# Kernel tuning notes

Measured on AMD Instinct MI355X. Metric: run time of the kernel, lower is better.

Reference implementation:

```python
import jax, jax.numpy as jnp
import numpy as np

N_NODES = 50000
N_EDGES = 800000
IN_FEATS = 256
OUT_FEATS = 64


def setup_inputs() -> dict:
    key = jax.random.key(0)
    k1, k2, k3, k4 = jax.random.split(key, 4)
    feat = jax.random.normal(k1, (N_NODES, IN_FEATS), dtype=jnp.float32)
    # xavier_uniform-like init for weight
    limit = float(np.sqrt(6.0 / (IN_FEATS + OUT_FEATS)))
    weight = jax.random.uniform(k2, (IN_FEATS, OUT_FEATS), dtype=jnp.float32,
                                minval=-limit, maxval=limit)
    bias = jnp.zeros((OUT_FEATS,), dtype=jnp.float32)
    src = jax.random.randint(k3, (N_EDGES,), 0, N_NODES, dtype=jnp.int32)
    dst = jax.random.randint(k4, (N_EDGES,), 0, N_NODES, dtype=jnp.int32)
    return {"feat": feat, "weight": weight, "bias": bias, "src": src, "dst": dst}


def reference(feat, weight, bias, src, dst):
    # GCN GraphConv with norm='both', edge_weight=None, activation=None.
    n = feat.shape[0]
    ones_e = jnp.ones(src.shape[0], dtype=feat.dtype)
    out_deg = jnp.clip(jax.ops.segment_sum(ones_e, src, num_segments=n), 1.0)
    in_deg = jnp.clip(jax.ops.segment_sum(ones_e, dst, num_segments=n), 1.0)

    # left/both pre-normalization by out-degree^{-1/2}
    feat_src = feat * (out_deg ** -0.5)[:, None]

    # lin_before_mp: in_feats (256) > out_feats (64) -> project first
    h = feat_src @ weight  # [N, out_feats]

    # copy_u + sum aggregation: gather from src, scatter-add to dst
    rst = jax.ops.segment_sum(h[src], dst, num_segments=n)  # [N, out_feats]

    # right/both post-normalization by in-degree^{-1/2}, then bias
    rst = rst * (in_deg ** -0.5)[:, None] + bias
    return rst
```

## Files before the change

kernel.cpp:

```cpp
#include <hip/hip_runtime.h>
#include <hip/hip_bf16.h>

#define N_NODES 50000
#define N_EDGES 800000
#define IN_F 256
#define OUT_F 64
#define NBUCKET 196
#define CAPB 6144
#define HCOPIES 32
#define EDGES_PER_COPY 25000
#define HWORDS 25000
#define PBLOCKS 200
#define EDGES_PER_PBLOCK 4000

using bf16x8 = __attribute__((ext_vector_type(8))) short;
using f32x4  = __attribute__((ext_vector_type(4))) float;

__global__ __launch_bounds__(1024)
void hist_kernel(const int* __restrict__ src, unsigned* __restrict__ scratch) {
    __shared__ unsigned lh[HWORDS];
    int tid = threadIdx.x, b = blockIdx.x;
    int e0 = b * EDGES_PER_COPY;
    for (int i = tid; i < HWORDS; i += 1024) lh[i] = 0;
    __syncthreads();
    for (int i = tid; i < EDGES_PER_COPY; i += 1024) {
        int id = src[e0 + i];
        atomicAdd(&lh[id >> 1], (id & 1) ? 0x10000u : 1u);
    }
    __syncthreads();
    unsigned* outp = scratch + (size_t)b * HWORDS;
    for (int i = tid; i < HWORDS; i += 1024) outp[i] = lh[i];
}

__global__ void reduce_kernel(const unsigned* __restrict__ scratch,
                              int* __restrict__ cnt_out) {
    int j = blockIdx.x * blockDim.x + threadIdx.x;
    if (j >= HWORDS) return;
    unsigned lo = 0, hi = 0;
    for (int k = 0; k < HCOPIES; ++k) {
        unsigned v = scratch[(size_t)k * HWORDS + j];
        lo += v & 0xFFFFu; hi += v >> 16;
    }
    cnt_out[2 * j] = (int)lo;
    cnt_out[2 * j + 1] = (int)hi;
}

__global__ __launch_bounds__(1024)
void partition_kernel(const int* __restrict__ src, const int* __restrict__ dst,
                      int* __restrict__ bucket_cursor, unsigned* __restrict__ recs) {
    __shared__ int lcnt[NBUCKET], lbase[NBUCKET];
    int tid = threadIdx.x;
    int e0 = blockIdx.x * EDGES_PER_PBLOCK;
    if (tid < NBUCKET) lcnt[tid] = 0;
    __syncthreads();
    unsigned rec[4]; int bkt[4], rnk[4];
#pragma unroll
    for (int j = 0; j < 4; ++j) {
        int i = j * 1024 + tid;
        bkt[j] = -1;
        if (i < EDGES_PER_PBLOCK) {
            int e = e0 + i;
            int s = src[e], d = dst[e];
            bkt[j] = d >> 8;
            rec[j] = (unsigned)s | ((unsigned)(d & 255) << 16);
            rnk[j] = atomicAdd(&lcnt[bkt[j]], 1);
        }
    }
    __syncthreads();
    if (tid < NBUCKET) lbase[tid] = atomicAdd(&bucket_cursor[tid * 16], lcnt[tid]);
    __syncthreads();
#pragma unroll
    for (int j = 0; j < 4; ++j) {
        if (bkt[j] >= 0) {
            int pos = lbase[bkt[j]] + rnk[j];
            if (pos < CAPB)
                recs[(size_t)bkt[j] * CAPB + pos] = rec[j];
        }
    }
}

__global__ __launch_bounds__(256)
void gemm_kernel(const float* __restrict__ feat, const float* __restrict__ weight,
                 const int* __restrict__ cnt_out, __hip_bfloat16* __restrict__ h) {
    __shared__ __align__(16) short Wt[64 * 256];
    int tid = threadIdx.x;

#pragma unroll
    for (int it = 0; it < 16; ++it) {
        int idx = it * 256 + tid;
        int k  = idx >> 4;
        int n4 = (idx & 15) * 4;
        float4 wv = *(const float4*)&weight[k * OUT_F + n4];
#pragma unroll
        for (int j = 0; j < 4; ++j) {
            int n = n4 + j;
            __hip_bfloat16 bv = __float2bfloat16((&wv.x)[j]);
            int byte = (n * 512 + k * 2) ^ ((n & 7) << 4);
            *(short*)((char*)Wt + byte) = *(short*)&bv;
        }
    }

    int lane = tid & 63, w = tid >> 6;
    int rowbase = blockIdx.x * 64 + w * 16;
    int arow = rowbase + (lane & 15);
    int arc = min(arow, N_NODES - 1);
    float sc = rsqrtf((float)max(cnt_out[arc], 1));
    const float* ap = &feat[arc * IN_F + (lane >> 4) * 8];
    __syncthreads();

    f32x4 acc[4];
#pragma unroll
    for (int c = 0; c < 4; ++c) acc[c] = (f32x4){0.f, 0.f, 0.f, 0.f};

#pragma unroll
    for (int ks = 0; ks < 8; ++ks) {
        float4 a0 = *(const float4*)(ap + ks * 32);
        float4 a1 = *(const float4*)(ap + ks * 32 + 4);
        bf16x8 af;
#pragma unroll
        for (int j = 0; j < 4; ++j) {
            __hip_bfloat16 b0 = __float2bfloat16((&a0.x)[j] * sc);
            __hip_bfloat16 b1 = __float2bfloat16((&a1.x)[j] * sc);
            af[j]     = *(short*)&b0;
            af[j + 4] = *(short*)&b1;
        }
        int kb = ks * 64 + (lane >> 4) * 16;
#pragma unroll
        for (int c = 0; c < 4; ++c) {
            int n = c * 16 + (lane & 15);
            int byte = (n * 512 + kb) ^ ((n & 7) << 4);
            bf16x8 bfv = *(const bf16x8*)((const char*)Wt + byte);
            acc[c] = __builtin_amdgcn_mfma_f32_16x16x32_bf16(af, bfv, acc[c], 0, 0, 0);
        }
    }

#pragma unroll
    for (int c = 0; c < 4; ++c) {
#pragma unroll
        for (int r = 0; r < 4; ++r) {
            int row = rowbase + (lane >> 4) * 4 + r;
            if (row < N_NODES)
                h[row * OUT_F + c * 16 + (lane & 15)] = __float2bfloat16(acc[c][r]);
        }
    }
}

__global__ __launch_bounds__(1024)
void aggregate_kernel(const __hip_bfloat16* __restrict__ h, const unsigned* __restrict__ recs,
                      const int* __restrict__ bucket_cursor,
                      const float* __restrict__ bias, float* __restrict__ out) {
    __shared__ int cnt[256], off[256], cur[256];
    __shared__ unsigned short order[CAPB];
    int tid = threadIdx.x, lane = tid & 63, w = tid >> 6;
    int b = blockIdx.x;
    if (tid < 256) { cnt[tid] = 0; cur[tid] = 0; }
    __syncthreads();
    size_t start = (size_t)b * CAPB;
    int n = min(bucket_cursor[b * 16], CAPB);

    for (int i = tid; i < n; i += 1024)
        atomicAdd(&cnt[(recs[start + i] >> 16) & 255u], 1);
    __syncthreads();

    if (tid < 256) off[tid] = cnt[tid];
    __syncthreads();
    for (int o = 1; o < 256; o <<= 1) {
        int y = (tid < 256 && tid >= o) ? off[tid - o] : 0;
        __syncthreads();
        if (tid < 256) off[tid] += y;
        __syncthreads();
    }

    for (int i = tid; i < n; i += 1024) {
        unsigned rec = recs[start + i];
        int dl = (rec >> 16) & 255u;
        int r = atomicAdd(&cur[dl], 1);
        int pos = off[dl] - cnt[dl] + r;
        order[pos] = (unsigned short)(rec & 0xFFFFu);
    }
    __syncthreads();

    float bv = bias[lane];
    int gbase = b * 256;
    for (int nd = w; nd < 256; nd += 16) {
        int g = gbase + nd;
        if (g >= N_NODES) continue;
        int m = cnt[nd];
        int s0 = off[nd] - m;
        float acc = 0.f;
        int k = 0;
        for (; k + 4 <= m; k += 4) {
            int a0 = order[s0 + k], a1 = order[s0 + k + 1];
            int a2 = order[s0 + k + 2], a3 = order[s0 + k + 3];
            acc += __bfloat162float(h[a0 * OUT_F + lane]) + __bfloat162float(h[a1 * OUT_F + lane])
                 + __bfloat162float(h[a2 * OUT_F + lane]) + __bfloat162float(h[a3 * OUT_F + lane]);
        }
        for (; k < m; ++k) acc += __bfloat162float(h[order[s0 + k] * OUT_F + lane]);
        float sc = rsqrtf((float)max(m, 1));
        out[g * OUT_F + lane] = fmaf(acc, sc, bv);
    }
}

extern "C" void kernel_launch(void* const* d_in, const int* in_sizes, int n_in,
                              void* d_out, int out_size, void* d_ws, size_t ws_size,
                              hipStream_t stream) {
    const float* feat   = (const float*)d_in[0];
    const float* weight = (const float*)d_in[1];
    const float* bias   = (const float*)d_in[2];
    const int*   src    = (const int*)d_in[3];
    const int*   dst    = (const int*)d_in[4];
    float* out = (float*)d_out;

    int* ws            = (int*)d_ws;
    int* cnt_out       = ws;
    int* bucket_cursor = ws + 50048;
    unsigned* scratch  = (unsigned*)(ws + 53248);
    unsigned* recs     = (unsigned*)(ws + 853248);
    __hip_bfloat16* h  = (__hip_bfloat16*)(ws + 2057472);

    hipMemsetAsync(bucket_cursor, 0, 3136 * sizeof(int), stream);

    hist_kernel<<<HCOPIES, 1024, 0, stream>>>(src, scratch);
    reduce_kernel<<<(HWORDS + 1023) / 1024, 1024, 0, stream>>>(scratch, cnt_out);
    partition_kernel<<<PBLOCKS, 1024, 0, stream>>>(src, dst, bucket_cursor, recs);
    gemm_kernel<<<(N_NODES + 63) / 64, 256, 0, stream>>>(feat, weight, cnt_out, h);
    aggregate_kernel<<<NBUCKET, 1024, 0, stream>>>(h, recs, bucket_cursor, bias, out);
}
```

Baseline: 163.5 us.

## Fuse degree reduce into histogram via global atomics and cache bucket records

Removes the separate reduce kernel and the per-copy scratch buffer. Each histogram block now atomically adds its packed 16-bit-pair counts directly into a global packed degree array, which the GEMM unpacks. The weight staging in the GEMM now writes 8 bf16 values per LDS store instead of scalar shorts. The aggregate kernel keeps its bucket records in registers, so recs is read once instead of twice. The costs are global atomic contention, wider uncoalesced weight reads, and a larger memset that now covers the packed counts.

Result: no change. 162.1 us (-0.8%).

```diff
diff --git a/kernel.cpp b/kernel.cpp
--- a/kernel.cpp
+++ b/kernel.cpp
@@ -17,7 +17,7 @@
 using f32x4  = __attribute__((ext_vector_type(4))) float;
 
 __global__ __launch_bounds__(1024)
-void hist_kernel(const int* __restrict__ src, unsigned* __restrict__ scratch) {
+void hist_kernel(const int* __restrict__ src, unsigned* __restrict__ cnt_out_packed) {
     __shared__ unsigned lh[HWORDS];
     int tid = threadIdx.x, b = blockIdx.x;
     int e0 = b * EDGES_PER_COPY;
@@ -28,21 +28,10 @@
         atomicAdd(&lh[id >> 1], (id & 1) ? 0x10000u : 1u);
     }
     __syncthreads();
-    unsigned* outp = scratch + (size_t)b * HWORDS;
-    for (int i = tid; i < HWORDS; i += 1024) outp[i] = lh[i];
-}
-
-__global__ void reduce_kernel(const unsigned* __restrict__ scratch,
-                              int* __restrict__ cnt_out) {
-    int j = blockIdx.x * blockDim.x + threadIdx.x;
-    if (j >= HWORDS) return;
-    unsigned lo = 0, hi = 0;
-    for (int k = 0; k < HCOPIES; ++k) {
-        unsigned v = scratch[(size_t)k * HWORDS + j];
-        lo += v & 0xFFFFu; hi += v >> 16;
-    }
-    cnt_out[2 * j] = (int)lo;
-    cnt_out[2 * j + 1] = (int)hi;
+    for (int i = tid; i < HWORDS; i += 1024) {
+        unsigned v = lh[i];
+        if (v) atomicAdd(&cnt_out_packed[i], v);
+    }
 }
 
 __global__ __launch_bounds__(1024)
@@ -81,30 +70,32 @@
 
 __global__ __launch_bounds__(256)
 void gemm_kernel(const float* __restrict__ feat, const float* __restrict__ weight,
-                 const int* __restrict__ cnt_out, __hip_bfloat16* __restrict__ h) {
+                 const unsigned* __restrict__ cnt_out_packed, __hip_bfloat16* __restrict__ h) {
     __shared__ __align__(16) short Wt[64 * 256];
     int tid = threadIdx.x;
 
 #pragma unroll
-    for (int it = 0; it < 16; ++it) {
-        int idx = it * 256 + tid;
-        int k  = idx >> 4;
-        int n4 = (idx & 15) * 4;
-        float4 wv = *(const float4*)&weight[k * OUT_F + n4];
-#pragma unroll
-        for (int j = 0; j < 4; ++j) {
-            int n = n4 + j;
-            __hip_bfloat16 bv = __float2bfloat16((&wv.x)[j]);
-            int byte = (n * 512 + k * 2) ^ ((n & 7) << 4);
-            *(short*)((char*)Wt + byte) = *(short*)&bv;
-        }
+    for (int it = 0; it < 8; ++it) {
+        int slot = it * 256 + tid;
+        int n  = slot & 63;
+        int k8 = slot >> 6;
+        bf16x8 v;
+#pragma unroll
+        for (int r = 0; r < 8; ++r) {
+            __hip_bfloat16 bv = __float2bfloat16(weight[(k8 * 8 + r) * OUT_F + n]);
+            v[r] = *(short*)&bv;
+        }
+        int byte = (n * 512 + k8 * 16) ^ ((n & 7) << 4);
+        *(bf16x8*)((char*)Wt + byte) = v;
     }
 
     int lane = tid & 63, w = tid >> 6;
     int rowbase = blockIdx.x * 64 + w * 16;
     int arow = rowbase + (lane & 15);
     int arc = min(arow, N_NODES - 1);
-    float sc = rsqrtf((float)max(cnt_out[arc], 1));
+    unsigned pw = cnt_out_packed[arc >> 1];
+    int deg = (arc & 1) ? (int)(pw >> 16) : (int)(pw & 0xFFFFu);
+    float sc = rsqrtf((float)max(deg, 1));
     const float* ap = &feat[arc * IN_F + (lane >> 4) * 8];
     __syncthreads();
 
@@ -158,8 +149,17 @@
     size_t start = (size_t)b * CAPB;
     int n = min(bucket_cursor[b * 16], CAPB);
 
-    for (int i = tid; i < n; i += 1024)
-        atomicAdd(&cnt[(recs[start + i] >> 16) & 255u], 1);
+    unsigned myrec[6];
+#pragma unroll
+    for (int j = 0; j < 6; ++j) {
+        int i = j * 1024 + tid;
+        myrec[j] = (i < n) ? recs[start + i] : 0xFFFFFFFFu;
+    }
+
+#pragma unroll
+    for (int j = 0; j < 6; ++j)
+        if (myrec[j] != 0xFFFFFFFFu)
+            atomicAdd(&cnt[(myrec[j] >> 16) & 255u], 1);
     __syncthreads();
 
     if (tid < 256) off[tid] = cnt[tid];
@@ -171,12 +171,13 @@
         __syncthreads();
     }
 
-    for (int i = tid; i < n; i += 1024) {
-        unsigned rec = recs[start + i];
-        int dl = (rec >> 16) & 255u;
-        int r = atomicAdd(&cur[dl], 1);
-        int pos = off[dl] - cnt[dl] + r;
-        order[pos] = (unsigned short)(rec & 0xFFFFu);
+#pragma unroll
+    for (int j = 0; j < 6; ++j) {
+        if (myrec[j] != 0xFFFFFFFFu) {
+            int dl = (myrec[j] >> 16) & 255u;
+            int r = atomicAdd(&cur[dl], 1);
+            order[off[dl] - cnt[dl] + r] = (unsigned short)(myrec[j] & 0xFFFFu);
+        }
     }
     __syncthreads();
 
@@ -211,18 +212,16 @@
     const int*   dst    = (const int*)d_in[4];
     float* out = (float*)d_out;
 
-    int* ws            = (int*)d_ws;
-    int* cnt_out       = ws;
-    int* bucket_cursor = ws + 50048;
-    unsigned* scratch  = (unsigned*)(ws + 53248);
-    unsigned* recs     = (unsigned*)(ws + 853248);
-    __hip_bfloat16* h  = (__hip_bfloat16*)(ws + 2057472);
-
-    hipMemsetAsync(bucket_cursor, 0, 3136 * sizeof(int), stream);
-
-    hist_kernel<<<HCOPIES, 1024, 0, stream>>>(src, scratch);
-    reduce_kernel<<<(HWORDS + 1023) / 1024, 1024, 0, stream>>>(scratch, cnt_out);
+    int* ws               = (int*)d_ws;
+    unsigned* cnt_packed  = (unsigned*)ws;
+    int* bucket_cursor    = ws + 25000;
+    unsigned* recs        = (unsigned*)(ws + 28160);
+    __hip_bfloat16* h     = (__hip_bfloat16*)(ws + 28160 + (size_t)NBUCKET * CAPB);
+
+    hipMemsetAsync(cnt_packed, 0, 28136 * sizeof(int), stream);
+
+    hist_kernel<<<HCOPIES, 1024, 0, stream>>>(src, cnt_packed);
     partition_kernel<<<PBLOCKS, 1024, 0, stream>>>(src, dst, bucket_cursor, recs);
-    gemm_kernel<<<(N_NODES + 63) / 64, 256, 0, stream>>>(feat, weight, cnt_out, h);
+    gemm_kernel<<<(N_NODES + 63) / 64, 256, 0, stream>>>(feat, weight, cnt_packed, h);
     aggregate_kernel<<<NBUCKET, 1024, 0, stream>>>(h, recs, bucket_cursor, bias, out);
 }
```
